# Kernel optimization log

Measured on AMD Instinct MI355X. Metric: run time of the kernel, lower is better.

## Reference

```python
import jax, jax.numpy as jnp
import numpy as np

D, H, L, FF, V, B, S = 512, 8, 6, 2048, 4096, 2, 4096
EPS = 1e-5

def _unit(v):
    return v / jnp.linalg.norm(v, axis=-1, keepdims=True)

def _unitelu(v):
    return jax.nn.elu(_unit(v))

def _ln(x, g, b):
    m = jnp.mean(x, axis=-1, keepdims=True)
    var = jnp.var(x, axis=-1, keepdims=True)
    return (x - m) * jax.lax.rsqrt(var + EPS) * g + b

def setup_inputs() -> dict:
    key = jax.random.key(0)
    ks = jax.random.split(key, 16)
    s = 0.02
    inp = {
        'input': jax.random.randint(ks[0], (B, S), 0, V),
        'emb': jax.random.normal(ks[1], (V, D)) * s,
        'Wq': jax.random.normal(ks[2], (L, D, D)) * s,
        'bq': jnp.zeros((L, D)),
        'Wk': jax.random.normal(ks[3], (L, D, D)) * s,
        'bk': jnp.zeros((L, D)),
        'Wv': jax.random.normal(ks[4], (L, D, D)) * s,
        'bv': jnp.zeros((L, D)),
        'Wo': jax.random.normal(ks[5], (L, D, D)) * s,
        'bo': jnp.zeros((L, D)),
        'W1': jax.random.normal(ks[6], (L, FF, D)) * s,
        'b1': jnp.zeros((L, FF)),
        'W2': jax.random.normal(ks[7], (L, D, FF)) * s,
        'b2': jnp.zeros((L, D)),
        'g2': jnp.ones((L, D)),
        'be2': jnp.zeros((L, D)),
        'Wfc': jax.random.normal(ks[8], (V, D)) * s,
        'bfc': jnp.zeros((V,)),
    }
    return inp

def reference(input, emb, Wq, bq, Wk, bk, Wv, bv, Wo, bo, W1, b1, W2, b2, g2, be2, Wfc, bfc):
    # h: [S, B, D] (seq-major, matching input.permute(1,0) then embedding)
    h = emb[input.T]
    for l in range(L):
        # linear kernelized attention: O(S * dh^2) per head, no SxS matrix
        k = _unitelu((h @ Wk[l].T + bk[l]).reshape(S, B, H, -1))  # [S,B,H,dh]
        v = (h @ Wv[l].T + bv[l]).reshape(S, B, H, -1)
        A = jnp.einsum('sbnq,sbnv->bnvq', k, v)                    # [B,H,dh,dh]
        q = _unit((h @ Wq[l].T + bq[l]).reshape(S, B, H, -1))
        o = jnp.einsum('sbnq,bnvq->sbnv', q, A).reshape(S, B, D)
        h = h + (o @ Wo[l].T + bo[l])
        f = jax.nn.relu(h @ W1[l].T + b1[l]) @ W2[l].T + b2[l]
        h = _ln(h + f, g2[l], be2[l])
    out = h @ Wfc.T + bfc          # [S, B, V]
    return out.transpose(1, 2, 0)  # [B, V, S]
```

## Files before the change

### kernel.cpp

```cpp
#include <hip/hip_runtime.h>
#include <hip/hip_bf16.h>

#define D_  512
#define H_  8
#define DH_ 64
#define L_  6
#define FF_ 2048
#define V_  4096
#define B_  2
#define S_  4096
#define SB_ (S_*B_)
#define DD_ ((size_t)D_*D_)
#define FD_ ((size_t)FF_*D_)

typedef unsigned short u16;
typedef unsigned int   u32;
typedef _Float16 f16;
typedef f16   f16x8 __attribute__((ext_vector_type(8)));
typedef float f32x4 __attribute__((ext_vector_type(4)));

__device__ __forceinline__ float us2f(u16 u){
  union { u32 i; float f; } c; c.i = ((u32)u) << 16; return c.f;
}
__device__ __forceinline__ u16 f2b(float f){
  union { float f; u32 i; } c; c.f = f;
  u32 x = c.i;
  x += 0x7FFF + ((x >> 16) & 1);
  return (u16)(x >> 16);
}
__device__ __forceinline__ float h2f(u16 u){
  union { u16 s; f16 h; } c; c.s = u; return (float)c.h;
}
__device__ __forceinline__ u16 f2h(float f){
  union { f16 h; u16 s; } c; c.h = (f16)f; return c.s;
}
__device__ __forceinline__ float ldf(const void* p, size_t i, int isbf){
  return isbf ? us2f(((const u16*)p)[i]) : ((const float*)p)[i];
}

typedef const __attribute__((address_space(1))) u32* gas_u32p;
typedef       __attribute__((address_space(3))) u32* las_u32p;
__device__ __forceinline__ void async16(const u16* g, u16* l){
  __builtin_amdgcn_global_load_lds((gas_u32p)(const void*)g, (las_u32p)(void*)l, 16, 0, 0);
}

__global__ __launch_bounds__(64) void detect_dtype(const void* emb, int* flag)
{
  const int t = threadIdx.x;
  u16 hw = ((const u16*)emb)[t];
  int e = (hw >> 7) & 0xFF;
  int ok = ((e > 96) && (e < 160)) || ((hw & 0x7FFF) == 0);
  unsigned long long m = __ballot(ok);
  if (t == 0) *flag = (__popcll(m) >= 56) ? 1 : 0;
}

__global__ __launch_bounds__(256) void cvt_layer(
    const void* Wq, const void* Wk, const void* Wv, const void* Wo,
    const void* W1, const void* W2, int l, u16* __restrict__ dst, const int* flagp)
{
  const int isbf = *flagp;
  const size_t i = ((size_t)blockIdx.x * 256 + threadIdx.x) * 4;
  const size_t n4 = 4 * DD_, nW1 = n4 + FD_, nTot = n4 + 2 * FD_;
  if (i >= nTot) return;
  const void* src; size_t off;
  if (i < n4) {
    const int wsel = (int)(i / DD_);
    src = (wsel == 0) ? Wq : (wsel == 1) ? Wk : (wsel == 2) ? Wv : Wo;
    off = (size_t)l * DD_ + (i - (size_t)wsel * DD_);
  } else if (i < nW1) { src = W1; off = (size_t)l * FD_ + (i - n4); }
  else                { src = W2; off = (size_t)l * FD_ + (i - nW1); }
  ushort4 o;
  if (isbf) {
    ushort4 u = *(const ushort4*)((const u16*)src + off);
    o = make_ushort4(f2h(us2f(u.x)), f2h(us2f(u.y)), f2h(us2f(u.z)), f2h(us2f(u.w)));
  } else {
    float4 f = *(const float4*)((const float*)src + off);
    o = make_ushort4(f2h(f.x), f2h(f.y), f2h(f.z), f2h(f.w));
  }
  *(ushort4*)&dst[i] = o;
}

__global__ __launch_bounds__(256) void cvt1(
    const void* src, u16* __restrict__ dst, size_t n, const int* flagp)
{
  const int isbf = *flagp;
  const size_t i = ((size_t)blockIdx.x * 256 + threadIdx.x) * 4;
  if (i >= n) return;
  ushort4 o;
  if (isbf) {
    ushort4 u = *(const ushort4*)((const u16*)src + i);
    o = make_ushort4(f2h(us2f(u.x)), f2h(us2f(u.y)), f2h(us2f(u.z)), f2h(us2f(u.w)));
  } else {
    float4 f = *(const float4*)((const float*)src + i);
    o = make_ushort4(f2h(f.x), f2h(f.y), f2h(f.z), f2h(f.w));
  }
  *(ushort4*)&dst[i] = o;
}

template<int ACT, int OUTMODE, int PRE>
__global__ __launch_bounds__(256) void gemm_mfma(
    const u16* __restrict__ A, const u16* __restrict__ Bm,
    int bstride, int boff,
    const void* bias, size_t bias_off,
    const float* __restrict__ res,
    float* __restrict__ Cf, u16* __restrict__ Cb,
    void* __restrict__ Cout, size_t out_base,
    int M, int N, int K, const int* flagp)
{
  __shared__ u16 tile[(PRE + 1) * 8192];
  const int t = threadIdx.x, lane = t & 63, w = t >> 6;
  const int bm = blockIdx.y << 7, bn = blockIdx.x << 7;
  const int wr = w >> 1, wc = w & 1;
  const int col = lane & 15, quad = lane >> 4;

  const int srow = w * 16 + (lane >> 2);
  const int skol = (lane & 3) << 3;
  const u16* ag0 = A + (size_t)(bm + srow) * K + skol;
  const u16* ag1 = A + (size_t)(bm + 64 + srow) * K + skol;
  const u16* bg0 = Bm + ((size_t)(bn + srow) * bstride + boff) * K + skol;
  const u16* bg1 = Bm + ((size_t)(bn + 64 + srow) * bstride + boff) * K + skol;
  u16* la0 = &tile[       w * 512];
  u16* la1 = &tile[2048 + w * 512];
  u16* lb0 = &tile[4096 + w * 512];
  u16* lb1 = &tile[6144 + w * 512];

  const int nt = K >> 5;

  #pragma unroll
  for (int p = 0; p < PRE; ++p) {
    const int k0 = p << 5, bo = p * 8192;
    async16(ag0 + k0, la0 + bo);
    async16(ag1 + k0, la1 + bo);
    async16(bg0 + k0, lb0 + bo);
    async16(bg1 + k0, lb1 + bo);
  }
  if (PRE >= 2) asm volatile("s_waitcnt vmcnt(4)" ::: "memory");
  else          asm volatile("s_waitcnt vmcnt(0)" ::: "memory");
  __builtin_amdgcn_s_barrier();
  asm volatile("" ::: "memory");

  f32x4 acc[4][4] = {};
  for (int t2 = 0; t2 < nt; ++t2) {
    if (t2 + PRE < nt) {
      const int k0 = (t2 + PRE) << 5;
      const int bo = ((t2 + PRE) % (PRE + 1)) * 8192;
      async16(ag0 + k0, la0 + bo);
      async16(ag1 + k0, la1 + bo);
      async16(bg0 + k0, lb0 + bo);
      async16(bg1 + k0, lb1 + bo);
    }
    const int cur = (t2 % (PRE + 1)) * 8192;
    f16x8 af[4], bf[4];
    #pragma unroll
    for (int i = 0; i < 4; i++)
      af[i] = *(const f16x8*)&tile[cur + (wr * 64 + i * 16 + col) * 32 + quad * 8];
    #pragma unroll
    for (int j = 0; j < 4; j++)
      bf[j] = *(const f16x8*)&tile[cur + 4096 + (wc * 64 + j * 16 + col) * 32 + quad * 8];
    #pragma unroll
    for (int i = 0; i < 4; i++)
      #pragma unroll
      for (int j = 0; j < 4; j++)
        acc[i][j] = __builtin_amdgcn_mfma_f32_16x16x32_f16(af[i], bf[j], acc[i][j], 0, 0, 0);
    if (PRE >= 2 && t2 + 2 < nt) asm volatile("s_waitcnt vmcnt(4)" ::: "memory");
    else                         asm volatile("s_waitcnt vmcnt(0)" ::: "memory");
    __builtin_amdgcn_s_barrier();
    asm volatile("" ::: "memory");
  }

  const int isbf = *flagp;
  if (OUTMODE == 4) {
    #pragma unroll
    for (int i = 0; i < 4; i++) {
      #pragma unroll
      for (int r = 0; r < 4; r++) {
        float v[4]; float ss = 0.f;
        #pragma unroll
        for (int j = 0; j < 4; j++) {
          const int n = bn + wc * 64 + j * 16 + col;
          v[j] = acc[i][j][r] + ldf(bias, bias_off + n, isbf);
          ss += v[j] * v[j];
        }
        ss += __shfl_xor(ss, 1); ss += __shfl_xor(ss, 2);
        ss += __shfl_xor(ss, 4); ss += __shfl_xor(ss, 8);
        const float inv = rsqrtf(fmaxf(ss, 1e-30f));
        const int m = bm + wr * 64 + i * 16 + quad * 4 + r;
        #pragma unroll
        for (int j = 0; j < 4; j++) {
          float u = v[j] * inv;
          if (ACT) u = (u > 0.f) ? u : expm1f(u);
          const int n = bn + wc * 64 + j * 16 + col;
          Cb[(size_t)m * N + n] = f2h(u);
        }
      }
    }
  } else {
    #pragma unroll
    for (int i = 0; i < 4; i++) {
      #pragma unroll
      for (int r = 0; r < 4; r++) {
        const int m = bm + wr * 64 + i * 16 + quad * 4 + r;
        #pragma unroll
        for (int j = 0; j < 4; j++) {
          const int n = bn + wc * 64 + j * 16 + col;
          float c = acc[i][j][r];
          if (OUTMODE == 3) c += ldf(bias, bias_off + m, isbf);
          else              c += ldf(bias, bias_off + n, isbf);
          if (res) c += res[(size_t)m * N + n];
          if (ACT == 1 && OUTMODE != 4) c = fmaxf(c, 0.f);
          if (OUTMODE == 0) {
            Cb[(size_t)m * N + n] = f2h(c);
          } else if (OUTMODE == 1) {
            Cf[(size_t)m * N + n] = c;
            Cb[(size_t)m * N + n] = f2h(c);
          } else {
            const size_t oi = out_base + (size_t)m * N + n;
            if (isbf) ((u16*)Cout)[oi] = f2b(c);
            else      ((float*)Cout)[oi] = c;
          }
        }
      }
    }
  }
}

__global__ __launch_bounds__(256) void gemm_qkv(
    const u16* __restrict__ A, const u16* __restrict__ Bm,
    const void* bq, const void* bk, const void* bv, size_t b_off,
    u16* __restrict__ qb, u16* __restrict__ kb, u16* __restrict__ vb,
    int K, const int* flagp)
{
  __shared__ u16 tile[3 * 8192];
  const int t = threadIdx.x, lane = t & 63, w = t >> 6;
  const int bm = blockIdx.y << 7, bn = blockIdx.x << 7;
  const int wr = w >> 1, wc = w & 1;
  const int col = lane & 15, quad = lane >> 4;

  const int srow = w * 16 + (lane >> 2);
  const int skol = (lane & 3) << 3;
  const u16* ag0 = A + (size_t)(bm + srow) * K + skol;
  const u16* ag1 = A + (size_t)(bm + 64 + srow) * K + skol;
  const u16* bg0 = Bm + (size_t)(bn + srow) * K + skol;
  const u16* bg1 = Bm + (size_t)(bn + 64 + srow) * K + skol;
  u16* la0 = &tile[       w * 512];
  u16* la1 = &tile[2048 + w * 512];
  u16* lb0 = &tile[4096 + w * 512];
  u16* lb1 = &tile[6144 + w * 512];

  const int nt = K >> 5;

  #pragma unroll
  for (int p = 0; p < 2; ++p) {
    const int k0 = p << 5, bo = p * 8192;
    async16(ag0 + k0, la0 + bo);
    async16(ag1 + k0, la1 + bo);
    async16(bg0 + k0, lb0 + bo);
    async16(bg1 + k0, lb1 + bo);
  }
  asm volatile("s_waitcnt vmcnt(4)" ::: "memory");
  __builtin_amdgcn_s_barrier();
  asm volatile("" ::: "memory");

  f32x4 acc[4][4] = {};
  for (int t2 = 0; t2 < nt; ++t2) {
    if (t2 + 2 < nt) {
      const int k0 = (t2 + 2) << 5;
      const int bo = ((t2 + 2) % 3) * 8192;
      async16(ag0 + k0, la0 + bo);
      async16(ag1 + k0, la1 + bo);
      async16(bg0 + k0, lb0 + bo);
      async16(bg1 + k0, lb1 + bo);
    }
    const int cur = (t2 % 3) * 8192;
    f16x8 af[4], bf[4];
    #pragma unroll
    for (int i = 0; i < 4; i++)
      af[i] = *(const f16x8*)&tile[cur + (wr * 64 + i * 16 + col) * 32 + quad * 8];
    #pragma unroll
    for (int j = 0; j < 4; j++)
      bf[j] = *(const f16x8*)&tile[cur + 4096 + (wc * 64 + j * 16 + col) * 32 + quad * 8];
    #pragma unroll
    for (int i = 0; i < 4; i++)
      #pragma unroll
      for (int j = 0; j < 4; j++)
        acc[i][j] = __builtin_amdgcn_mfma_f32_16x16x32_f16(af[i], bf[j], acc[i][j], 0, 0, 0);
    if (t2 + 2 < nt) asm volatile("s_waitcnt vmcnt(4)" ::: "memory");
    else             asm volatile("s_waitcnt vmcnt(0)" ::: "memory");
    __builtin_amdgcn_s_barrier();
    asm volatile("" ::: "memory");
  }

  const int isbf = *flagp;
  const int nbase = bn + wc * 64;
  const int sel = nbase >> 9;
  const int nl0 = nbase & 511;
  u16* outp = (sel == 0) ? qb : (sel == 1) ? kb : vb;
  const void* bias = (sel == 0) ? bq : (sel == 1) ? bk : bv;

  if (sel < 2) {
    #pragma unroll
    for (int i = 0; i < 4; i++) {
      #pragma unroll
      for (int r = 0; r < 4; r++) {
        float v[4]; float ss = 0.f;
        #pragma unroll
        for (int j = 0; j < 4; j++) {
          const int nl = nl0 + j * 16 + col;
          v[j] = acc[i][j][r] + ldf(bias, b_off + nl, isbf);
          ss += v[j] * v[j];
        }
        ss += __shfl_xor(ss, 1); ss += __shfl_xor(ss, 2);
        ss += __shfl_xor(ss, 4); ss += __shfl_xor(ss, 8);
        const float inv = rsqrtf(fmaxf(ss, 1e-30f));
        const int m = bm + wr * 64 + i * 16 + quad * 4 + r;
        #pragma unroll
        for (int j = 0; j < 4; j++) {
          float u = v[j] * inv;
          if (sel == 1) u = (u > 0.f) ? u : expm1f(u);
          outp[(size_t)m * 512 + nl0 + j * 16 + col] = f2h(u);
        }
      }
    }
  } else {
    #pragma unroll
    for (int i = 0; i < 4; i++)
      #pragma unroll
      for (int r = 0; r < 4; r++) {
        const int m = bm + wr * 64 + i * 16 + quad * 4 + r;
        #pragma unroll
        for (int j = 0; j < 4; j++) {
          const int nl = nl0 + j * 16 + col;
          outp[(size_t)m * 512 + nl] = f2h(acc[i][j][r] + ldf(bias, b_off + nl, isbf));
        }
      }
  }
}

#define KT_ 136
__global__ __launch_bounds__(256) void attn_acc_mfma(
    const u16* __restrict__ kbuf, const u16* __restrict__ vbuf,
    float* __restrict__ Apart)
{
  __shared__ u16 ktr[64 * KT_];
  __shared__ u16 vtr[64 * KT_];
  const int bh = blockIdx.x;
  const int b  = bh >> 3, n = bh & 7;
  const int s0 = blockIdx.y << 7;
  const int t = threadIdx.x, lane = t & 63, w = t >> 6;
  const int col = lane & 15, quad = lane >> 4;

  #pragma unroll
  for (int u = 0; u < 8; u++) {
    const int flat = u * 256 + t;
    const int row = flat >> 4, q4 = (flat & 15) << 2;
    const size_t g = ((size_t)(s0 + row) * B_ + b) * D_ + n * 64 + q4;
    ushort4 kk = *(const ushort4*)&kbuf[g];
    ushort4 vv = *(const ushort4*)&vbuf[g];
    ktr[(q4+0)*KT_ + row] = kk.x; ktr[(q4+1)*KT_ + row] = kk.y;
    ktr[(q4+2)*KT_ + row] = kk.z; ktr[(q4+3)*KT_ + row] = kk.w;
    vtr[(q4+0)*KT_ + row] = vv.x; vtr[(q4+1)*KT_ + row] = vv.y;
    vtr[(q4+2)*KT_ + row] = vv.z; vtr[(q4+3)*KT_ + row] = vv.w;
  }
  __syncthreads();

  f32x4 acc[4] = {};
  #pragma unroll
  for (int ks = 0; ks < 4; ks++) {
    const int k0 = ks * 32;
    f16x8 af = *(const f16x8*)&vtr[(w * 16 + col) * KT_ + k0 + quad * 8];
    #pragma unroll
    for (int j = 0; j < 4; j++) {
      f16x8 bf = *(const f16x8*)&ktr[(j * 16 + col) * KT_ + k0 + quad * 8];
      acc[j] = __builtin_amdgcn_mfma_f32_16x16x32_f16(af, bf, acc[j], 0, 0, 0);
    }
  }
  float* Ap = Apart + ((size_t)blockIdx.y * 16 + bh) * 4096;
  #pragma unroll
  for (int j = 0; j < 4; j++)
    #pragma unroll
    for (int r = 0; r < 4; r++) {
      const int vi = w * 16 + quad * 4 + r, qi = j * 16 + col;
      Ap[vi * 64 + qi] = acc[j][r];
    }
}

__global__ __launch_bounds__(256) void reduce_A(
    const float* __restrict__ Apart, u16* __restrict__ Ah)
{
  const int i = blockIdx.x * 256 + threadIdx.x;
  const int bh = i >> 12, idx = i & 4095;
  float s = 0.f;
  #pragma unroll
  for (int p = 0; p < 32; p++)
    s += Apart[((size_t)p * 16 + bh) * 4096 + idx];
  Ah[i] = f2h(s);
}

__global__ __launch_bounds__(256) void attn_apply_mfma(
    u16* __restrict__ qo, const u16* __restrict__ Ah)
{
  const int bh = blockIdx.x;
  const int b = bh >> 3, n = bh & 7;
  const int s0 = blockIdx.y << 7;
  const int t = threadIdx.x, lane = t & 63, w = t >> 6;
  const int col = lane & 15, quad = lane >> 4;

  const u16* Ab_ = Ah + (size_t)bh * 4096;
  f16x8 bf[4][2];
  #pragma unroll
  for (int j = 0; j < 4; j++)
    #pragma unroll
    for (int ks = 0; ks < 2; ks++)
      bf[j][ks] = *(const f16x8*)&Ab_[(j * 16 + col) * 64 + ks * 32 + quad * 8];

  const int srow_base = s0 + w * 32;
  f32x4 acc[2][4] = {};
  #pragma unroll
  for (int i = 0; i < 2; i++) {
    const int s = srow_base + i * 16 + col;
    const u16* qp = qo + ((size_t)s * B_ + b) * D_ + n * 64;
    f16x8 af0 = *(const f16x8*)&qp[quad * 8];
    f16x8 af1 = *(const f16x8*)&qp[32 + quad * 8];
    #pragma unroll
    for (int j = 0; j < 4; j++) {
      acc[i][j] = __builtin_amdgcn_mfma_f32_16x16x32_f16(af0, bf[j][0], acc[i][j], 0, 0, 0);
      acc[i][j] = __builtin_amdgcn_mfma_f32_16x16x32_f16(af1, bf[j][1], acc[i][j], 0, 0, 0);
    }
  }
  #pragma unroll
  for (int i = 0; i < 2; i++)
    #pragma unroll
    for (int r = 0; r < 4; r++) {
      const int s = srow_base + i * 16 + quad * 4 + r;
      u16* op = qo + ((size_t)s * B_ + b) * D_ + n * 64;
      #pragma unroll
      for (int j = 0; j < 4; j++)
        op[j * 16 + col] = f2h(acc[i][j][r]);
    }
}

__global__ __launch_bounds__(256) void ln_k(
    float* __restrict__ h, u16* __restrict__ hb,
    const void* g, size_t g_off, const void* be, size_t be_off, const int* flagp)
{
  const int isbf = *flagp;
  const int m = blockIdx.x, t = threadIdx.x;
  float* p = h + (size_t)m * D_;
  const float x0 = p[t], x1 = p[t + 256];
  __shared__ float red[4];
  float s = x0 + x1;
  #pragma unroll
  for (int off = 32; off >= 1; off >>= 1) s += __shfl_xor(s, off);
  if ((t & 63) == 0) red[t >> 6] = s;
  __syncthreads();
  const float mean = (red[0] + red[1] + red[2] + red[3]) * (1.f / 512.f);
  const float d0 = x0 - mean, d1 = x1 - mean;
  float s2 = d0 * d0 + d1 * d1;
  #pragma unroll
  for (int off = 32; off >= 1; off >>= 1) s2 += __shfl_xor(s2, off);
  __syncthreads();
  if ((t & 63) == 0) red[t >> 6] = s2;
  __syncthreads();
  const float var = (red[0] + red[1] + red[2] + red[3]) * (1.f / 512.f);
  const float sc = rsqrtf(var + 1e-5f);
  const float y0 = d0 * sc * ldf(g, g_off + t, isbf)       + ldf(be, be_off + t, isbf);
  const float y1 = d1 * sc * ldf(g, g_off + t + 256, isbf) + ldf(be, be_off + t + 256, isbf);
  p[t] = y0;       p[t + 256] = y1;
  hb[(size_t)m * D_ + t] = f2h(y0);
  hb[(size_t)m * D_ + t + 256] = f2h(y1);
}

__global__ __launch_bounds__(512) void embed_k(
    const int* __restrict__ inp, const void* emb,
    float* __restrict__ h, u16* __restrict__ hb, const int* flagp)
{
  const int isbf = *flagp;
  const int m = blockIdx.x, t = threadIdx.x;
  const int s = m >> 1, b = m & 1;
  const int tok = inp[b * S_ + s];
  const float v = ldf(emb, (size_t)tok * D_ + t, isbf);
  h[(size_t)m * D_ + t] = v;
  hb[(size_t)m * D_ + t] = f2h(v);
}

extern "C" void kernel_launch(void* const* d_in, const int* in_sizes, int n_in,
                              void* d_out, int out_size, void* d_ws, size_t ws_size,
                              hipStream_t stream) {
  const int*  inp = (const int*) d_in[0];
  const void* emb = d_in[1];
  const void* Wq  = d_in[2];
  const void* bq  = d_in[3];
  const void* Wk  = d_in[4];
  const void* bk  = d_in[5];
  const void* Wv  = d_in[6];
  const void* bv  = d_in[7];
  const void* Wo  = d_in[8];
  const void* bo  = d_in[9];
  const void* W1  = d_in[10];
  const void* b1  = d_in[11];
  const void* W2  = d_in[12];
  const void* b2  = d_in[13];
  const void* g2  = d_in[14];
  const void* be2 = d_in[15];
  const void* Wfc = d_in[16];
  const void* bfc = d_in[17];

  char* ws = (char*)d_ws;
  float* h     = (float*)(ws);
  u16*   hb    = (u16*)  (ws + 16777216);
  u16*   qb    = (u16*)  (ws + 25165824);
  u16*   kb    = (u16*)  (ws + 33554432);
  u16*   vb    = (u16*)  (ws + 41943040);
  u16*   mid   = qb;
  float* Apart = (float*)(ws + 58720256);
  u16*   Ah16  = (u16*)  (ws + 67108864);
  u16*   Wc    = (u16*)  (ws + 67239936);
  int*   flag  = (int*)  (ws + 73531392);

  detect_dtype<<<1, 64, 0, stream>>>(emb, flag);
  embed_k<<<SB_, 512, 0, stream>>>(inp, emb, h, hb, flag);

  const dim3 gQ(D_ / 128, SB_ / 128);
  const dim3 gQKV(3 * D_ / 128, SB_ / 128);
  const dim3 gF(FF_ / 128, SB_ / 128);
  const dim3 gFC(S_ / 128, V_ / 128);
  const dim3 gAT(B_ * H_, S_ / 128);

  for (int l = 0; l < L_; l++) {
    cvt_layer<<<3072, 256, 0, stream>>>(Wq, Wk, Wv, Wo, W1, W2, l, Wc, flag);

    gemm_qkv<<<gQKV, 256, 0, stream>>>(hb, Wc, bq, bk, bv, (size_t)l*D_, qb, kb, vb, D_, flag);

    attn_acc_mfma<<<gAT, 256, 0, stream>>>(kb, vb, Apart);
    reduce_A<<<256, 256, 0, stream>>>(Apart, Ah16);
    attn_apply_mfma<<<gAT, 256, 0, stream>>>(qb, Ah16);

    gemm_mfma<0,1,2><<<gQ, 256, 0, stream>>>(qb, Wc + 3*DD_,   1, 0, bo, (size_t)l*D_,  h, h, hb, nullptr, 0, SB_, D_, D_, flag);
    gemm_mfma<1,0,1><<<gF, 256, 0, stream>>>(hb, Wc + 4*DD_,   1, 0, b1, (size_t)l*FF_, nullptr, nullptr, mid, nullptr, 0, SB_, FF_, D_, flag);
    gemm_mfma<0,1,2><<<gQ, 256, 0, stream>>>(mid, Wc + 4*DD_ + FD_, 1, 0, b2, (size_t)l*D_, h, h, hb, nullptr, 0, SB_, D_, FF_, flag);
    ln_k<<<SB_, 256, 0, stream>>>(h, hb, g2, (size_t)l*D_, be2, (size_t)l*D_, flag);
  }

  cvt1<<<2048, 256, 0, stream>>>(Wfc, Wc, (size_t)V_ * D_, flag);
  gemm_mfma<0,3,1><<<gFC, 256, 0, stream>>>(Wc, hb, 2, 0, bfc, 0, nullptr, nullptr, nullptr, d_out, 0,                 V_, S_, D_, flag);
  gemm_mfma<0,3,1><<<gFC, 256, 0, stream>>>(Wc, hb, 2, 1, bfc, 0, nullptr, nullptr, nullptr, d_out, (size_t)V_ * S_, V_, S_, D_, flag);
}
```

Before: 1.565 ms.

## Batch weight conversion, swizzle LDS tiles, deepen GEMM prefetch pipeline

```diff
diff --git a/kernel.cpp b/kernel.cpp
--- a/kernel.cpp
+++ b/kernel.cpp
@@ -12,6 +12,7 @@
 #define SB_ (S_*B_)
 #define DD_ ((size_t)D_*D_)
 #define FD_ ((size_t)FF_*D_)
+#define NTOT_ (4*DD_ + 2*FD_)
 
 typedef unsigned short u16;
 typedef unsigned int   u32;
@@ -54,21 +55,31 @@
   if (t == 0) *flag = (__popcll(m) >= 56) ? 1 : 0;
 }
 
-__global__ __launch_bounds__(256) void cvt_layer(
+__global__ __launch_bounds__(256) void cvt_all(
     const void* Wq, const void* Wk, const void* Wv, const void* Wo,
-    const void* W1, const void* W2, int l, u16* __restrict__ dst, const int* flagp)
+    const void* W1, const void* W2, const void* Wfc,
+    u16* __restrict__ dstAll, u16* __restrict__ dstFC, const int* flagp)
 {
   const int isbf = *flagp;
+  const size_t total6 = 6 * NTOT_;
   const size_t i = ((size_t)blockIdx.x * 256 + threadIdx.x) * 4;
-  const size_t n4 = 4 * DD_, nW1 = n4 + FD_, nTot = n4 + 2 * FD_;
-  if (i >= nTot) return;
-  const void* src; size_t off;
-  if (i < n4) {
-    const int wsel = (int)(i / DD_);
-    src = (wsel == 0) ? Wq : (wsel == 1) ? Wk : (wsel == 2) ? Wv : Wo;
-    off = (size_t)l * DD_ + (i - (size_t)wsel * DD_);
-  } else if (i < nW1) { src = W1; off = (size_t)l * FD_ + (i - n4); }
-  else                { src = W2; off = (size_t)l * FD_ + (i - nW1); }
+  const void* src; size_t off; u16* dst;
+  if (i < total6) {
+    const int l = (int)(i / NTOT_);
+    const size_t r = i - (size_t)l * NTOT_;
+    const size_t n4 = 4 * DD_, nW1 = n4 + FD_;
+    if (r < n4) {
+      const int wsel = (int)(r / DD_);
+      src = (wsel == 0) ? Wq : (wsel == 1) ? Wk : (wsel == 2) ? Wv : Wo;
+      off = (size_t)l * DD_ + (r - (size_t)wsel * DD_);
+    } else if (r < nW1) { src = W1; off = (size_t)l * FD_ + (r - n4); }
+    else                { src = W2; off = (size_t)l * FD_ + (r - nW1); }
+    dst = dstAll + i;
+  } else {
+    const size_t j = i - total6;
+    if (j >= (size_t)V_ * D_) return;
+    src = Wfc; off = j; dst = dstFC + j;
+  }
   ushort4 o;
   if (isbf) {
     ushort4 u = *(const ushort4*)((const u16*)src + off);
@@ -77,24 +88,7 @@
     float4 f = *(const float4*)((const float*)src + off);
     o = make_ushort4(f2h(f.x), f2h(f.y), f2h(f.z), f2h(f.w));
   }
-  *(ushort4*)&dst[i] = o;
-}
-
-__global__ __launch_bounds__(256) void cvt1(
-    const void* src, u16* __restrict__ dst, size_t n, const int* flagp)
-{
-  const int isbf = *flagp;
-  const size_t i = ((size_t)blockIdx.x * 256 + threadIdx.x) * 4;
-  if (i >= n) return;
-  ushort4 o;
-  if (isbf) {
-    ushort4 u = *(const ushort4*)((const u16*)src + i);
-    o = make_ushort4(f2h(us2f(u.x)), f2h(us2f(u.y)), f2h(us2f(u.z)), f2h(us2f(u.w)));
-  } else {
-    float4 f = *(const float4*)((const float*)src + i);
-    o = make_ushort4(f2h(f.x), f2h(f.y), f2h(f.z), f2h(f.w));
-  }
-  *(ushort4*)&dst[i] = o;
+  *(ushort4*)dst = o;
 }
 
 template<int ACT, int OUTMODE, int PRE>
@@ -114,7 +108,7 @@
   const int col = lane & 15, quad = lane >> 4;
 
   const int srow = w * 16 + (lane >> 2);
-  const int skol = (lane & 3) << 3;
+  const int skol = (((lane & 3) ^ ((lane >> 3) & 3)) << 3);
   const u16* ag0 = A + (size_t)(bm + srow) * K + skol;
   const u16* ag1 = A + (size_t)(bm + 64 + srow) * K + skol;
   const u16* bg0 = Bm + ((size_t)(bn + srow) * bstride + boff) * K + skol;
@@ -134,10 +128,13 @@
     async16(bg0 + k0, lb0 + bo);
     async16(bg1 + k0, lb1 + bo);
   }
-  if (PRE >= 2) asm volatile("s_waitcnt vmcnt(4)" ::: "memory");
-  else          asm volatile("s_waitcnt vmcnt(0)" ::: "memory");
+  if      (PRE >= 3) asm volatile("s_waitcnt vmcnt(8)" ::: "memory");
+  else if (PRE == 2) asm volatile("s_waitcnt vmcnt(4)" ::: "memory");
+  else               asm volatile("s_waitcnt vmcnt(0)" ::: "memory");
   __builtin_amdgcn_s_barrier();
   asm volatile("" ::: "memory");
+
+  const int rswz = ((col >> 1) & 3);
 
   f32x4 acc[4][4] = {};
   for (int t2 = 0; t2 < nt; ++t2) {
@@ -153,71 +150,52 @@
     f16x8 af[4], bf[4];
     #pragma unroll
     for (int i = 0; i < 4; i++)
-      af[i] = *(const f16x8*)&tile[cur + (wr * 64 + i * 16 + col) * 32 + quad * 8];
+      af[i] = *(const f16x8*)&tile[cur + (wr * 64 + i * 16 + col) * 32 + ((quad ^ rswz) * 8)];
     #pragma unroll
     for (int j = 0; j < 4; j++)
-      bf[j] = *(const f16x8*)&tile[cur + 4096 + (wc * 64 + j * 16 + col) * 32 + quad * 8];
+      bf[j] = *(const f16x8*)&tile[cur + 4096 + (wc * 64 + j * 16 + col) * 32 + ((quad ^ rswz) * 8)];
     #pragma unroll
     for (int i = 0; i < 4; i++)
       #pragma unroll
       for (int j = 0; j < 4; j++)
         acc[i][j] = __builtin_amdgcn_mfma_f32_16x16x32_f16(af[i], bf[j], acc[i][j], 0, 0, 0);
-    if (PRE >= 2 && t2 + 2 < nt) asm volatile("s_waitcnt vmcnt(4)" ::: "memory");
-    else                         asm volatile("s_waitcnt vmcnt(0)" ::: "memory");
+    if (PRE >= 3) {
+      if      (t2 + 3 < nt) asm volatile("s_waitcnt vmcnt(8)" ::: "memory");
+      else if (t2 + 2 < nt) asm volatile("s_waitcnt vmcnt(4)" ::: "memory");
+      else                  asm volatile("s_waitcnt vmcnt(0)" ::: "memory");
+    } else if (PRE == 2) {
+      if (t2 + 2 < nt) asm volatile("s_waitcnt vmcnt(4)" ::: "memory");
+      else             asm volatile("s_waitcnt vmcnt(0)" ::: "memory");
+    } else {
+      asm volatile("s_waitcnt vmcnt(0)" ::: "memory");
+    }
     __builtin_amdgcn_s_barrier();
     asm volatile("" ::: "memory");
   }
 
   const int isbf = *flagp;
-  if (OUTMODE == 4) {
-    #pragma unroll
-    for (int i = 0; i < 4; i++) {
+  #pragma unroll
+  for (int i = 0; i < 4; i++) {
+    #pragma unroll
+    for (int r = 0; r < 4; r++) {
+      const int m = bm + wr * 64 + i * 16 + quad * 4 + r;
       #pragma unroll
-      for (int r = 0; r < 4; r++) {
-        float v[4]; float ss = 0.f;
-        #pragma unroll
-        for (int j = 0; j < 4; j++) {
-          const int n = bn + wc * 64 + j * 16 + col;
-          v[j] = acc[i][j][r] + ldf(bias, bias_off + n, isbf);
-          ss += v[j] * v[j];
-        }
-        ss += __shfl_xor(ss, 1); ss += __shfl_xor(ss, 2);
-        ss += __shfl_xor(ss, 4); ss += __shfl_xor(ss, 8);
-        const float inv = rsqrtf(fmaxf(ss, 1e-30f));
-        const int m = bm + wr * 64 + i * 16 + quad * 4 + r;
-        #pragma unroll
-        for (int j = 0; j < 4; j++) {
-          float u = v[j] * inv;
-          if (ACT) u = (u > 0.f) ? u : expm1f(u);
-          const int n = bn + wc * 64 + j * 16 + col;
-          Cb[(size_t)m * N + n] = f2h(u);
-        }
-      }
-    }
-  } else {
-    #pragma unroll
-    for (int i = 0; i < 4; i++) {
-      #pragma unroll
-      for (int r = 0; r < 4; r++) {
-        const int m = bm + wr * 64 + i * 16 + quad * 4 + r;
-        #pragma unroll
-        for (int j = 0; j < 4; j++) {
-          const int n = bn + wc * 64 + j * 16 + col;
-          float c = acc[i][j][r];
-          if (OUTMODE == 3) c += ldf(bias, bias_off + m, isbf);
-          else              c += ldf(bias, bias_off + n, isbf);
-          if (res) c += res[(size_t)m * N + n];
-          if (ACT == 1 && OUTMODE != 4) c = fmaxf(c, 0.f);
-          if (OUTMODE == 0) {
-            Cb[(size_t)m * N + n] = f2h(c);
-          } else if (OUTMODE == 1) {
-            Cf[(size_t)m * N + n] = c;
-            Cb[(size_t)m * N + n] = f2h(c);
-          } else {
-            const size_t oi = out_base + (size_t)m * N + n;
-            if (isbf) ((u16*)Cout)[oi] = f2b(c);
-            else      ((float*)Cout)[oi] = c;
-          }
+      for (int j = 0; j < 4; j++) {
+        const int n = bn + wc * 64 + j * 16 + col;
+        float c = acc[i][j][r];
+        if (OUTMODE == 3) c += ldf(bias, bias_off + m, isbf);
+        else              c += ldf(bias, bias_off + n, isbf);
+        if (res) c += res[(size_t)m * N + n];
+        if (ACT == 1) c = fmaxf(c, 0.f);
+        if (OUTMODE == 0) {
+          Cb[(size_t)m * N + n] = f2h(c);
+        } else if (OUTMODE == 1) {
+          Cf[(size_t)m * N + n] = c;
+          Cb[(size_t)m * N + n] = f2h(c);
+        } else {
+          const size_t oi = out_base + (size_t)m * N + n;
+          if (isbf) ((u16*)Cout)[oi] = f2b(c);
+          else      ((float*)Cout)[oi] = c;
         }
       }
     }
@@ -237,7 +215,7 @@
   const int col = lane & 15, quad = lane >> 4;
 
   const int srow = w * 16 + (lane >> 2);
-  const int skol = (lane & 3) << 3;
+  const int skol = (((lane & 3) ^ ((lane >> 3) & 3)) << 3);
   const u16* ag0 = A + (size_t)(bm + srow) * K + skol;
   const u16* ag1 = A + (size_t)(bm + 64 + srow) * K + skol;
   const u16* bg0 = Bm + (size_t)(bn + srow) * K + skol;
@@ -260,6 +238,8 @@
   asm volatile("s_waitcnt vmcnt(4)" ::: "memory");
   __builtin_amdgcn_s_barrier();
   asm volatile("" ::: "memory");
+
+  const int rswz = ((col >> 1) & 3);
 
   f32x4 acc[4][4] = {};
   for (int t2 = 0; t2 < nt; ++t2) {
@@ -275,10 +255,10 @@
     f16x8 af[4], bf[4];
     #pragma unroll
     for (int i = 0; i < 4; i++)
-      af[i] = *(const f16x8*)&tile[cur + (wr * 64 + i * 16 + col) * 32 + quad * 8];
+      af[i] = *(const f16x8*)&tile[cur + (wr * 64 + i * 16 + col) * 32 + ((quad ^ rswz) * 8)];
     #pragma unroll
     for (int j = 0; j < 4; j++)
-      bf[j] = *(const f16x8*)&tile[cur + 4096 + (wc * 64 + j * 16 + col) * 32 + quad * 8];
+      bf[j] = *(const f16x8*)&tile[cur + 4096 + (wc * 64 + j * 16 + col) * 32 + ((quad ^ rswz) * 8)];
     #pragma unroll
     for (int i = 0; i < 4; i++)
       #pragma unroll
@@ -514,10 +494,12 @@
   u16*   mid   = qb;
   float* Apart = (float*)(ws + 58720256);
   u16*   Ah16  = (u16*)  (ws + 67108864);
-  u16*   Wc    = (u16*)  (ws + 67239936);
-  int*   flag  = (int*)  (ws + 73531392);
+  u16*   WcAll = (u16*)  (ws + 67239936);
+  u16*   WcFC  = (u16*)  (ws + 104988672);
+  int*   flag  = (int*)  (ws + 109182976);
 
   detect_dtype<<<1, 64, 0, stream>>>(emb, flag);
+  cvt_all<<<20480, 256, 0, stream>>>(Wq, Wk, Wv, Wo, W1, W2, Wfc, WcAll, WcFC, flag);
   embed_k<<<SB_, 512, 0, stream>>>(inp, emb, h, hb, flag);
 
   const dim3 gQ(D_ / 128, SB_ / 128);
@@ -527,21 +509,20 @@
   const dim3 gAT(B_ * H_, S_ / 128);
 
   for (int l = 0; l < L_; l++) {
-    cvt_layer<<<3072, 256, 0, stream>>>(Wq, Wk, Wv, Wo, W1, W2, l, Wc, flag);
-
-    gemm_qkv<<<gQKV, 256, 0, stream>>>(hb, Wc, bq, bk, bv, (size_t)l*D_, qb, kb, vb, D_, flag);
+    u16* Wcl = WcAll + (size_t)l * NTOT_;
+
+    gemm_qkv<<<gQKV, 256, 0, stream>>>(hb, Wcl, bq, bk, bv, (size_t)l*D_, qb, kb, vb, D_, flag);
 
     attn_acc_mfma<<<gAT, 256, 0, stream>>>(kb, vb, Apart);
     reduce_A<<<256, 256, 0, stream>>>(Apart, Ah16);
     attn_apply_mfma<<<gAT, 256, 0, stream>>>(qb, Ah16);
 
-    gemm_mfma<0,1,2><<<gQ, 256, 0, stream>>>(qb, Wc + 3*DD_,   1, 0, bo, (size_t)l*D_,  h, h, hb, nullptr, 0, SB_, D_, D_, flag);
-    gemm_mfma<1,0,1><<<gF, 256, 0, stream>>>(hb, Wc + 4*DD_,   1, 0, b1, (size_t)l*FF_, nullptr, nullptr, mid, nullptr, 0, SB_, FF_, D_, flag);
-    gemm_mfma<0,1,2><<<gQ, 256, 0, stream>>>(mid, Wc + 4*DD_ + FD_, 1, 0, b2, (size_t)l*D_, h, h, hb, nullptr, 0, SB_, D_, FF_, flag);
+    gemm_mfma<0,1,3><<<gQ, 256, 0, stream>>>(qb, Wcl + 3*DD_,   1, 0, bo, (size_t)l*D_,  h, h, hb, nullptr, 0, SB_, D_, D_, flag);
+    gemm_mfma<1,0,2><<<gF, 256, 0, stream>>>(hb, Wcl + 4*DD_,   1, 0, b1, (size_t)l*FF_, nullptr, nullptr, mid, nullptr, 0, SB_, FF_, D_, flag);
+    gemm_mfma<0,1,3><<<gQ, 256, 0, stream>>>(mid, Wcl + 4*DD_ + FD_, 1, 0, b2, (size_t)l*D_, h, h, hb, nullptr, 0, SB_, D_, FF_, flag);
     ln_k<<<SB_, 256, 0, stream>>>(h, hb, g2, (size_t)l*D_, be2, (size_t)l*D_, flag);
   }
 
-  cvt1<<<2048, 256, 0, stream>>>(Wfc, Wc, (size_t)V_ * D_, flag);
-  gemm_mfma<0,3,1><<<gFC, 256, 0, stream>>>(Wc, hb, 2, 0, bfc, 0, nullptr, nullptr, nullptr, d_out, 0,                 V_, S_, D_, flag);
-  gemm_mfma<0,3,1><<<gFC, 256, 0, stream>>>(Wc, hb, 2, 1, bfc, 0, nullptr, nullptr, nullptr, d_out, (size_t)V_ * S_, V_, S_, D_, flag);
-}
+  gemm_mfma<0,3,2><<<gFC, 256, 0, stream>>>(WcFC, hb, 2, 0, bfc, 0, nullptr, nullptr, nullptr, d_out, 0,                 V_, S_, D_, flag);
+  gemm_mfma<0,3,2><<<gFC, 256, 0, stream>>>(WcFC, hb, 2, 1, bfc, 0, nullptr, nullptr, nullptr, d_out, (size_t)V_ * S_, V_, S_, D_, flag);
+}
```

New measurement: 1.511 ms. 1.04x faster.
